# Kernel tuning notes

Hardware: AMD Instinct MI355X
Metric: run time of the kernel (lower is better)

Reference implementation:

```python
import jax, jax.numpy as jnp
import numpy as np

VOCAB, EMBED, HIDDEN, NCLS = 50257, 64, 64, 5
B, S = 4096, 512
BN_EPS = 1e-5


def setup_inputs() -> dict:
    key = jax.random.key(0)
    ks = jax.random.split(key, 10)
    x = jax.random.randint(ks[0], (B, S), 0, VOCAB, dtype=jnp.int64 if jax.config.jax_enable_x64 else jnp.int32)
    emb = jax.random.normal(ks[1], (VOCAB, EMBED), dtype=jnp.float32)
    emb = emb.at[0].set(0.0)  # padding_idx=0
    s = 1.0 / np.sqrt(HIDDEN)
    W_ih = jax.random.uniform(ks[2], (HIDDEN, EMBED), minval=-s, maxval=s, dtype=jnp.float32)
    W_hh = jax.random.uniform(ks[3], (HIDDEN, HIDDEN), minval=-s, maxval=s, dtype=jnp.float32)
    b_ih = jax.random.uniform(ks[4], (HIDDEN,), minval=-s, maxval=s, dtype=jnp.float32)
    b_hh = jax.random.uniform(ks[5], (HIDDEN,), minval=-s, maxval=s, dtype=jnp.float32)
    gamma = jnp.ones((HIDDEN,), dtype=jnp.float32)
    beta = jnp.zeros((HIDDEN,), dtype=jnp.float32)
    sf = 1.0 / np.sqrt(HIDDEN)
    W_fc = jax.random.uniform(ks[6], (NCLS, HIDDEN), minval=-sf, maxval=sf, dtype=jnp.float32)
    b_fc = jax.random.uniform(ks[7], (NCLS,), minval=-sf, maxval=sf, dtype=jnp.float32)
    return {"x": x, "emb": emb, "W_ih": W_ih, "W_hh": W_hh, "b_ih": b_ih,
            "b_hh": b_hh, "gamma": gamma, "beta": beta, "W_fc": W_fc, "b_fc": b_fc}


def reference(x, emb, W_ih, W_hh, b_ih, b_hh, gamma, beta, W_fc, b_fc):
    # embedding gather: [B, S, E]
    xe = emb[x]
    # precompute input projection once: [B, S, H] -> scan over time as [S, B, H]
    xp = jnp.einsum('bse,he->bsh', xe, W_ih) + b_ih + b_hh
    xp_t = jnp.swapaxes(xp, 0, 1)

    def step(h, xt):
        h = jnp.tanh(xt + h @ W_hh.T)
        return h, None

    h0 = jnp.zeros((x.shape[0], HIDDEN), dtype=xp.dtype)
    h_n, _ = jax.lax.scan(step, h0, xp_t)

    # BatchNorm1d (training-mode math: batch stats, biased variance)
    mean = jnp.mean(h_n, axis=0)
    var = jnp.mean((h_n - mean) ** 2, axis=0)
    h_bn = (h_n - mean) * jax.lax.rsqrt(var + BN_EPS) * gamma + beta
    # dropout is identity in eval / deterministic reference
    logits = h_bn @ W_fc.T + b_fc  # [B, 5]
    return logits
```

## Files before the change

kernel.cpp:

```cpp
#include <hip/hip_runtime.h>

typedef unsigned short u16;
typedef __attribute__((ext_vector_type(8))) short bf16x8;
typedef __attribute__((ext_vector_type(4))) float f32x4;
typedef __attribute__((ext_vector_type(4))) u16 u16x4;

constexpr int BATCH  = 4096;
constexpr int SEQ    = 512;
constexpr int HID    = 64;
constexpr int EMB_N4 = 50257 * 64 / 4;

__device__ __forceinline__ float bf2f(u16 u) {
  union { unsigned int i; float f; } c; c.i = ((unsigned int)u) << 16; return c.f;
}
__device__ __forceinline__ u16 f2bf(float f) {
  union { float f; unsigned int i; } c; c.f = f;
  unsigned int u = c.i;
  u += 0x7fffu + ((u >> 16) & 1u);
  return (u16)(u >> 16);
}

#define MFMA16(a, b, c) __builtin_amdgcn_mfma_f32_16x16x32_bf16(a, b, c, 0, 0, 0)

__global__ __launch_bounds__(256) void prep_kernel(
    const float4* __restrict__ emb4, const float* __restrict__ Wih,
    const float* __restrict__ Whh, u16x4* __restrict__ emb_bf4,
    u16* __restrict__ wih_hi, u16* __restrict__ whh_hi, u16* __restrict__ whh_lo,
    float* __restrict__ bn_acc)
{
  int gid = blockIdx.x * 256 + threadIdx.x;
  if (gid < EMB_N4) {
    float4 v = emb4[gid];
    u16x4 o;
    o.x = f2bf(v.x); o.y = f2bf(v.y); o.z = f2bf(v.z); o.w = f2bf(v.w);
    emb_bf4[gid] = o;
  } else if (gid < EMB_N4 + 1024) {
    int i0 = (gid - EMB_N4) * 4;
    #pragma unroll
    for (int k = 0; k < 4; ++k) {
      int i = i0 + k;
      wih_hi[i] = f2bf(Wih[i]);
      float w = Whh[i];
      u16 hi = f2bf(w);
      whh_hi[i] = hi;
      whh_lo[i] = f2bf(w - bf2f(hi));
    }
  } else if (gid < EMB_N4 + 1024 + 128) {
    bn_acc[gid - (EMB_N4 + 1024)] = 0.f;
  }
}

__global__ __launch_bounds__(256, 1) void rnn_scan_kernel(
    const int* __restrict__ xx, const u16* __restrict__ emb_bf,
    const u16* __restrict__ wih_hi, const u16* __restrict__ whh_hi,
    const u16* __restrict__ whh_lo,
    const float* __restrict__ b_ih, const float* __restrict__ b_hh,
    float* __restrict__ hT , float* __restrict__ bn_acc)
{
  __shared__ u16 hbuf[2 * 2048];
  const int tid = threadIdx.x;
  const int w = tid >> 6;
  const int L = tid & 63;
  const int n = L & 15;
  const int q = L >> 4;
  const int R0 = blockIdx.x << 4;
  const int row  = R0 + n;
  const int feat = (w << 4) + n;

  ((int4*)hbuf)[tid] = int4{0, 0, 0, 0};

  bf16x8 Bih0 = *(const bf16x8*)(wih_hi + feat * 64 +      8 * q);
  bf16x8 Bih1 = *(const bf16x8*)(wih_hi + feat * 64 + 32 + 8 * q);
  bf16x8 Bh0  = *(const bf16x8*)(whh_hi + feat * 64 +      8 * q);
  bf16x8 Bh1  = *(const bf16x8*)(whh_hi + feat * 64 + 32 + 8 * q);
  bf16x8 Bl0  = *(const bf16x8*)(whh_lo + feat * 64 +      8 * q);
  bf16x8 Bl1  = *(const bf16x8*)(whh_lo + feat * 64 + 32 + 8 * q);
  const float bias = b_ih[feat] + b_hh[feat];

  const int r0off = n * 64 + (((0 + q) ^ (n & 7)) << 3);
  const int r1off = n * 64 + (((4 + q) ^ (n & 7)) << 3);
  const int cwbase = (w << 1) + (n >> 3);

  const int4* x4 = (const int4*)(xx + row * SEQ);
  int4 K1 = x4[1];

  bf16x8 e0[4], e1[4];
  {
    int4 K0 = x4[0];
    const int id0[4] = {K0.x, K0.y, K0.z, K0.w};
    #pragma unroll
    for (int u = 0; u < 4; ++u) {
      const u16* eb = emb_bf + (long)id0[u] * 64 + 8 * q;
      e0[u] = *(const bf16x8*)(eb);
      e1[u] = *(const bf16x8*)(eb + 32);
    }
  }

  __syncthreads();

  for (int t = 0; t < SEQ / 4; ++t) {
    int4 K2 = x4[(t + 2 < SEQ / 4) ? t + 2 : SEQ / 4 - 1];
    const int nid[4] = {K1.x, K1.y, K1.z, K1.w};
    const bool lastt = (t == SEQ / 4 - 1);

    #pragma unroll
    for (int u = 0; u < 4; ++u) {
      const int p = u & 1;
      const u16* hb = hbuf + p * 2048;
      bf16x8 ah0 = *(const bf16x8*)(hb + r0off);
      bf16x8 ah1 = *(const bf16x8*)(hb + r1off);
      bf16x8 al0 = *(const bf16x8*)(hb + 1024 + r0off);
      bf16x8 al1 = *(const bf16x8*)(hb + 1024 + r1off);

      f32x4 C1 = {bias, bias, bias, bias};
      C1 = MFMA16(e0[u], Bih0, C1);
      C1 = MFMA16(e1[u], Bih1, C1);

      {
        const u16* eb = emb_bf + (long)nid[u] * 64 + 8 * q;
        e0[u] = *(const bf16x8*)(eb);
        e1[u] = *(const bf16x8*)(eb + 32);
      }

      f32x4 Cx = {0.f, 0.f, 0.f, 0.f};
      f32x4 Cy = {0.f, 0.f, 0.f, 0.f};
      f32x4 Cz = {0.f, 0.f, 0.f, 0.f};
      Cx = MFMA16(ah0, Bh0, Cx);  Cx = MFMA16(al0, Bh0, Cx);
      Cy = MFMA16(ah1, Bh1, Cy);  Cy = MFMA16(al1, Bh1, Cy);
      Cz = MFMA16(ah0, Bl0, Cz);  Cz = MFMA16(ah1, Bl1, Cz);

      u16* wb = hbuf + (p ^ 1) * 2048;
      float th4[4];
      #pragma unroll
      for (int r = 0; r < 4; ++r) {
        float v = (C1[r] + Cx[r]) + (Cy[r] + Cz[r]);
        float ex = __builtin_amdgcn_exp2f(2.8853900817779268f * v);
        float th = fmaf(-2.0f, __builtin_amdgcn_rcpf(ex + 1.0f), 1.0f);
        th4[r] = th;
        const int mw = (q << 2) + r;
        const int off = mw * 64 + ((cwbase ^ (mw & 7)) << 3) + (n & 7);
        unsigned int tb = __float_as_uint(th);
        wb[off] = (u16)(tb >> 16);
        wb[1024 + off] = (u16)(__float_as_uint(th - __uint_as_float(tb & 0xffff0000u)) >> 16);
      }

      if (u == 3 && lastt) {
        float s1 = 0.f, s2 = 0.f;
        #pragma unroll
        for (int r = 0; r < 4; ++r) {
          hT[feat * BATCH + R0 + (q << 2) + r] = th4[r];
          s1 += th4[r];
          s2 = fmaf(th4[r], th4[r], s2);
        }
        s1 += __shfl_xor(s1, 16, 64);  s2 += __shfl_xor(s2, 16, 64);
        s1 += __shfl_xor(s1, 32, 64);  s2 += __shfl_xor(s2, 32, 64);
        if (q == 0) {
          atomicAdd(bn_acc + feat, s1);
          atomicAdd(bn_acc + 64 + feat, s2);
        }
      }

      asm volatile("s_waitcnt lgkmcnt(0)\n\ts_barrier" ::: "memory");
    }
    K1 = K2;
  }
}

__global__ __launch_bounds__(256) void head_kernel(
    const float* __restrict__ hT, const float* __restrict__ bn_acc,
    const float* __restrict__ gamma, const float* __restrict__ beta,
    const float* __restrict__ Wfc, const float* __restrict__ bfc,
    float* __restrict__ out)
{
  __shared__ float sc[64], sh[64];
  const int tid = threadIdx.x;
  if (tid < 64) {
    float mean = bn_acc[tid] * (1.0f / BATCH);
    float var  = bn_acc[64 + tid] * (1.0f / BATCH) - mean * mean;
    float inv  = rsqrtf(var + 1e-5f);
    float s    = gamma[tid] * inv;
    sc[tid] = s;
    sh[tid] = beta[tid] - mean * s;
  }
  __syncthreads();
  const int b = blockIdx.x * 256 + tid;
  float acc[5];
  #pragma unroll
  for (int c = 0; c < 5; ++c) acc[c] = bfc[c];
  for (int j = 0; j < HID; ++j) {
    float hv  = hT[j * BATCH + b];
    float hat = fmaf(hv, sc[j], sh[j]);
    #pragma unroll
    for (int c = 0; c < 5; ++c) acc[c] = fmaf(hat, Wfc[c * 64 + j], acc[c]);
  }
  #pragma unroll
  for (int c = 0; c < 5; ++c) out[b * 5 + c] = acc[c];
}

extern "C" void kernel_launch(void* const* d_in, const int* in_sizes, int n_in,
                              void* d_out, int out_size, void* d_ws, size_t ws_size,
                              hipStream_t stream)
{
  const int*   x     = (const int*)d_in[0];
  const float* emb   = (const float*)d_in[1];
  const float* W_ih  = (const float*)d_in[2];
  const float* W_hh  = (const float*)d_in[3];
  const float* b_ih  = (const float*)d_in[4];
  const float* b_hh  = (const float*)d_in[5];
  const float* gamma = (const float*)d_in[6];
  const float* beta  = (const float*)d_in[7];
  const float* W_fc  = (const float*)d_in[8];
  const float* b_fc  = (const float*)d_in[9];

  char* ws = (char*)d_ws;
  float* hT     = (float*)ws;
  float* bn_acc = (float*)(ws + 1048576);
  u16*   emb_bf = (u16*)(ws + 1049088);
  u16*   wih_hi = (u16*)(ws + 7481984);
  u16*   whh_hi = (u16*)(ws + 7490176);
  u16*   whh_lo = (u16*)(ws + 7498368);

  const int prep_items = EMB_N4 + 1024 + 128;
  prep_kernel<<<dim3((prep_items + 255) / 256), dim3(256), 0, stream>>>(
      (const float4*)emb, W_ih, W_hh, (u16x4*)emb_bf, wih_hi, whh_hi, whh_lo, bn_acc);
  rnn_scan_kernel<<<dim3(BATCH / 16), dim3(256), 0, stream>>>(
      x, emb_bf, wih_hi, whh_hi, whh_lo, b_ih, b_hh, hT, bn_acc);
  head_kernel<<<dim3(BATCH / 256), dim3(256), 0, stream>>>(
      hT, bn_acc, gamma, beta, W_fc, b_fc, (float*)d_out);
}
```

Measured before the change: 251.5 us.

## Run RNN scan in one wave with register-resident fp16 hidden state

Restructures the recurrent scan so that a single 64-lane wavefront owns all 64 hidden features for 16 batch rows. The transposed MFMA output layout is fed back directly as the next step's B operand, which removes the LDS hidden-state buffer and the per-timestep barrier. It also replaces the split bf16 hi/lo operands with single fp16 operands and folds the tanh exp2 scaling into the weights and bias. This halves the MFMA count per step and removes the shared-memory traffic on the critical path. The costs are lower hidden-state precision, now fp16 without error compensation, and only one wave per block, which reduces latency hiding across the 256 blocks.

```diff
diff --git a/kernel.cpp b/kernel.cpp
--- a/kernel.cpp
+++ b/kernel.cpp
@@ -1,102 +1,90 @@
 #include <hip/hip_runtime.h>
 
-typedef unsigned short u16;
-typedef __attribute__((ext_vector_type(8))) short bf16x8;
+typedef _Float16 f16;
+typedef __attribute__((ext_vector_type(4))) _Float16 f16x4;
+typedef __attribute__((ext_vector_type(8))) _Float16 f16x8;
 typedef __attribute__((ext_vector_type(4))) float f32x4;
-typedef __attribute__((ext_vector_type(4))) u16 u16x4;
 
 constexpr int BATCH  = 4096;
 constexpr int SEQ    = 512;
 constexpr int HID    = 64;
 constexpr int EMB_N4 = 50257 * 64 / 4;
-
-__device__ __forceinline__ float bf2f(u16 u) {
-  union { unsigned int i; float f; } c; c.i = ((unsigned int)u) << 16; return c.f;
-}
-__device__ __forceinline__ u16 f2bf(float f) {
-  union { float f; unsigned int i; } c; c.f = f;
-  unsigned int u = c.i;
-  u += 0x7fffu + ((u >> 16) & 1u);
-  return (u16)(u >> 16);
-}
-
-#define MFMA16(a, b, c) __builtin_amdgcn_mfma_f32_16x16x32_bf16(a, b, c, 0, 0, 0)
+constexpr float LOG2E2 = 2.8853900817779268f;
+
+#define MFMA_K32(a, b, c) __builtin_amdgcn_mfma_f32_16x16x32_f16(a, b, c, 0, 0, 0)
 
 __global__ __launch_bounds__(256) void prep_kernel(
     const float4* __restrict__ emb4, const float* __restrict__ Wih,
-    const float* __restrict__ Whh, u16x4* __restrict__ emb_bf4,
-    u16* __restrict__ wih_hi, u16* __restrict__ whh_hi, u16* __restrict__ whh_lo,
-    float* __restrict__ bn_acc)
+    const float* __restrict__ Whh, f16x4* __restrict__ emb_f4,
+    f16* __restrict__ wih_f, f16* __restrict__ whh_f, float* __restrict__ bn_acc)
 {
   int gid = blockIdx.x * 256 + threadIdx.x;
   if (gid < EMB_N4) {
     float4 v = emb4[gid];
-    u16x4 o;
-    o.x = f2bf(v.x); o.y = f2bf(v.y); o.z = f2bf(v.z); o.w = f2bf(v.w);
-    emb_bf4[gid] = o;
+    f16x4 o = {(f16)v.x, (f16)v.y, (f16)v.z, (f16)v.w};
+    emb_f4[gid] = o;
   } else if (gid < EMB_N4 + 1024) {
     int i0 = (gid - EMB_N4) * 4;
     #pragma unroll
     for (int k = 0; k < 4; ++k) {
       int i = i0 + k;
-      wih_hi[i] = f2bf(Wih[i]);
-      float w = Whh[i];
-      u16 hi = f2bf(w);
-      whh_hi[i] = hi;
-      whh_lo[i] = f2bf(w - bf2f(hi));
+      wih_f[i] = (f16)(Wih[i] * LOG2E2);
+      whh_f[i] = (f16)(Whh[i] * LOG2E2);
     }
   } else if (gid < EMB_N4 + 1024 + 128) {
     bn_acc[gid - (EMB_N4 + 1024)] = 0.f;
   }
 }
 
-__global__ __launch_bounds__(256, 1) void rnn_scan_kernel(
-    const int* __restrict__ xx, const u16* __restrict__ emb_bf,
-    const u16* __restrict__ wih_hi, const u16* __restrict__ whh_hi,
-    const u16* __restrict__ whh_lo,
+__global__ __launch_bounds__(64, 1) void rnn_scan_kernel(
+    const int* __restrict__ xx, const f16* __restrict__ emb,
+    const f16* __restrict__ wih, const f16* __restrict__ whh,
     const float* __restrict__ b_ih, const float* __restrict__ b_hh,
     float* __restrict__ hT , float* __restrict__ bn_acc)
 {
-  __shared__ u16 hbuf[2 * 2048];
-  const int tid = threadIdx.x;
-  const int w = tid >> 6;
-  const int L = tid & 63;
+  const int L = threadIdx.x;
   const int n = L & 15;
   const int q = L >> 4;
   const int R0 = blockIdx.x << 4;
-  const int row  = R0 + n;
-  const int feat = (w << 4) + n;
-
-  ((int4*)hbuf)[tid] = int4{0, 0, 0, 0};
-
-  bf16x8 Bih0 = *(const bf16x8*)(wih_hi + feat * 64 +      8 * q);
-  bf16x8 Bih1 = *(const bf16x8*)(wih_hi + feat * 64 + 32 + 8 * q);
-  bf16x8 Bh0  = *(const bf16x8*)(whh_hi + feat * 64 +      8 * q);
-  bf16x8 Bh1  = *(const bf16x8*)(whh_hi + feat * 64 + 32 + 8 * q);
-  bf16x8 Bl0  = *(const bf16x8*)(whh_lo + feat * 64 +      8 * q);
-  bf16x8 Bl1  = *(const bf16x8*)(whh_lo + feat * 64 + 32 + 8 * q);
-  const float bias = b_ih[feat] + b_hh[feat];
-
-  const int r0off = n * 64 + (((0 + q) ^ (n & 7)) << 3);
-  const int r1off = n * 64 + (((4 + q) ^ (n & 7)) << 3);
-  const int cwbase = (w << 1) + (n >> 3);
-
-  const int4* x4 = (const int4*)(xx + row * SEQ);
+
+  f16x8 Wi[4][2], Wp[4][2];
+  f32x4 bias[4];
+  #pragma unroll
+  for (int f = 0; f < 4; ++f) {
+    const f16* wr = whh + (16 * f + n) * 64;
+    #pragma unroll
+    for (int h = 0; h < 2; ++h) {
+      f16x4 lo = *(const f16x4*)(wr + 32 * h + 4 * q);
+      f16x4 hi = *(const f16x4*)(wr + 32 * h + 16 + 4 * q);
+      Wp[f][h] = __builtin_shufflevector(lo, hi, 0, 1, 2, 3, 4, 5, 6, 7);
+    }
+    const f16* wi = wih + (16 * f + n) * 64;
+    Wi[f][0] = *(const f16x8*)(wi + 8 * q);
+    Wi[f][1] = *(const f16x8*)(wi + 32 + 8 * q);
+    float4 bi = *(const float4*)(b_ih + 16 * f + 4 * q);
+    float4 bh = *(const float4*)(b_hh + 16 * f + 4 * q);
+    f32x4 b = {(bi.x + bh.x) * LOG2E2, (bi.y + bh.y) * LOG2E2,
+               (bi.z + bh.z) * LOG2E2, (bi.w + bh.w) * LOG2E2};
+    bias[f] = b;
+  }
+
+  f16x8 hB01 = {0, 0, 0, 0, 0, 0, 0, 0};
+  f16x8 hB23 = {0, 0, 0, 0, 0, 0, 0, 0};
+
+  const int4* x4 = (const int4*)(xx + (R0 + n) * SEQ);
   int4 K1 = x4[1];
 
-  bf16x8 e0[4], e1[4];
+  f16x8 e0[4], e1[4];
   {
     int4 K0 = x4[0];
     const int id0[4] = {K0.x, K0.y, K0.z, K0.w};
     #pragma unroll
     for (int u = 0; u < 4; ++u) {
-      const u16* eb = emb_bf + (long)id0[u] * 64 + 8 * q;
-      e0[u] = *(const bf16x8*)(eb);
-      e1[u] = *(const bf16x8*)(eb + 32);
-    }
-  }
-
-  __syncthreads();
+      const f16* eb = emb + (long)id0[u] * 64 + 8 * q;
+      e0[u] = *(const f16x8*)(eb);
+      e1[u] = *(const f16x8*)(eb + 32);
+    }
+  }
 
   for (int t = 0; t < SEQ / 4; ++t) {
     int4 K2 = x4[(t + 2 < SEQ / 4) ? t + 2 : SEQ / 4 - 1];
@@ -105,62 +93,67 @@
 
     #pragma unroll
     for (int u = 0; u < 4; ++u) {
-      const int p = u & 1;
-      const u16* hb = hbuf + p * 2048;
-      bf16x8 ah0 = *(const bf16x8*)(hb + r0off);
-      bf16x8 ah1 = *(const bf16x8*)(hb + r1off);
-      bf16x8 al0 = *(const bf16x8*)(hb + 1024 + r0off);
-      bf16x8 al1 = *(const bf16x8*)(hb + 1024 + r1off);
-
-      f32x4 C1 = {bias, bias, bias, bias};
-      C1 = MFMA16(e0[u], Bih0, C1);
-      C1 = MFMA16(e1[u], Bih1, C1);
+      f32x4 D0 = MFMA_K32(Wi[0][0], e0[u], bias[0]);
+      f32x4 D1 = MFMA_K32(Wi[1][0], e0[u], bias[1]);
+      f32x4 D2 = MFMA_K32(Wi[2][0], e0[u], bias[2]);
+      f32x4 D3 = MFMA_K32(Wi[3][0], e0[u], bias[3]);
+      D0 = MFMA_K32(Wi[0][1], e1[u], D0);
+      D1 = MFMA_K32(Wi[1][1], e1[u], D1);
+      D2 = MFMA_K32(Wi[2][1], e1[u], D2);
+      D3 = MFMA_K32(Wi[3][1], e1[u], D3);
 
       {
-        const u16* eb = emb_bf + (long)nid[u] * 64 + 8 * q;
-        e0[u] = *(const bf16x8*)(eb);
-        e1[u] = *(const bf16x8*)(eb + 32);
+        const f16* eb = emb + (long)nid[u] * 64 + 8 * q;
+        e0[u] = *(const f16x8*)(eb);
+        e1[u] = *(const f16x8*)(eb + 32);
       }
 
-      f32x4 Cx = {0.f, 0.f, 0.f, 0.f};
-      f32x4 Cy = {0.f, 0.f, 0.f, 0.f};
-      f32x4 Cz = {0.f, 0.f, 0.f, 0.f};
-      Cx = MFMA16(ah0, Bh0, Cx);  Cx = MFMA16(al0, Bh0, Cx);
-      Cy = MFMA16(ah1, Bh1, Cy);  Cy = MFMA16(al1, Bh1, Cy);
-      Cz = MFMA16(ah0, Bl0, Cz);  Cz = MFMA16(ah1, Bl1, Cz);
-
-      u16* wb = hbuf + (p ^ 1) * 2048;
-      float th4[4];
+      D0 = MFMA_K32(Wp[0][0], hB01, D0);
+      D1 = MFMA_K32(Wp[1][0], hB01, D1);
+      D2 = MFMA_K32(Wp[2][0], hB01, D2);
+      D3 = MFMA_K32(Wp[3][0], hB01, D3);
+      D0 = MFMA_K32(Wp[0][1], hB23, D0);
+      D1 = MFMA_K32(Wp[1][1], hB23, D1);
+      D2 = MFMA_K32(Wp[2][1], hB23, D2);
+      D3 = MFMA_K32(Wp[3][1], hB23, D3);
+
+      float th[4][4];
       #pragma unroll
       for (int r = 0; r < 4; ++r) {
-        float v = (C1[r] + Cx[r]) + (Cy[r] + Cz[r]);
-        float ex = __builtin_amdgcn_exp2f(2.8853900817779268f * v);
-        float th = fmaf(-2.0f, __builtin_amdgcn_rcpf(ex + 1.0f), 1.0f);
-        th4[r] = th;
-        const int mw = (q << 2) + r;
-        const int off = mw * 64 + ((cwbase ^ (mw & 7)) << 3) + (n & 7);
-        unsigned int tb = __float_as_uint(th);
-        wb[off] = (u16)(tb >> 16);
-        wb[1024 + off] = (u16)(__float_as_uint(th - __uint_as_float(tb & 0xffff0000u)) >> 16);
+        float e0f = __builtin_amdgcn_exp2f(D0[r]);
+        float e1f = __builtin_amdgcn_exp2f(D1[r]);
+        float e2f = __builtin_amdgcn_exp2f(D2[r]);
+        float e3f = __builtin_amdgcn_exp2f(D3[r]);
+        th[0][r] = fmaf(-2.0f, __builtin_amdgcn_rcpf(e0f + 1.0f), 1.0f);
+        th[1][r] = fmaf(-2.0f, __builtin_amdgcn_rcpf(e1f + 1.0f), 1.0f);
+        th[2][r] = fmaf(-2.0f, __builtin_amdgcn_rcpf(e2f + 1.0f), 1.0f);
+        th[3][r] = fmaf(-2.0f, __builtin_amdgcn_rcpf(e3f + 1.0f), 1.0f);
+        hB01[r]     = (f16)th[0][r];
+        hB01[4 + r] = (f16)th[1][r];
+        hB23[r]     = (f16)th[2][r];
+        hB23[4 + r] = (f16)th[3][r];
       }
 
-      if (u == 3 && lastt) {
-        float s1 = 0.f, s2 = 0.f;
+      if (lastt && u == 3) {
         #pragma unroll
-        for (int r = 0; r < 4; ++r) {
-          hT[feat * BATCH + R0 + (q << 2) + r] = th4[r];
-          s1 += th4[r];
-          s2 = fmaf(th4[r], th4[r], s2);
-        }
-        s1 += __shfl_xor(s1, 16, 64);  s2 += __shfl_xor(s2, 16, 64);
-        s1 += __shfl_xor(s1, 32, 64);  s2 += __shfl_xor(s2, 32, 64);
-        if (q == 0) {
-          atomicAdd(bn_acc + feat, s1);
-          atomicAdd(bn_acc + 64 + feat, s2);
+        for (int f = 0; f < 4; ++f) {
+          #pragma unroll
+          for (int r = 0; r < 4; ++r) {
+            float v = th[f][r];
+            const int feat = 16 * f + 4 * q + r;
+            hT[feat * BATCH + R0 + n] = v;
+            float s1 = v, s2 = v * v;
+            s1 += __shfl_xor(s1, 1, 64);  s2 += __shfl_xor(s2, 1, 64);
+            s1 += __shfl_xor(s1, 2, 64);  s2 += __shfl_xor(s2, 2, 64);
+            s1 += __shfl_xor(s1, 4, 64);  s2 += __shfl_xor(s2, 4, 64);
+            s1 += __shfl_xor(s1, 8, 64);  s2 += __shfl_xor(s2, 8, 64);
+            if (n == 0) {
+              atomicAdd(bn_acc + feat, s1);
+              atomicAdd(bn_acc + 64 + feat, s2);
+            }
+          }
         }
       }
-
-      asm volatile("s_waitcnt lgkmcnt(0)\n\ts_barrier" ::: "memory");
     }
     K1 = K2;
   }
@@ -215,16 +208,15 @@
   char* ws = (char*)d_ws;
   float* hT     = (float*)ws;
   float* bn_acc = (float*)(ws + 1048576);
-  u16*   emb_bf = (u16*)(ws + 1049088);
-  u16*   wih_hi = (u16*)(ws + 7481984);
-  u16*   whh_hi = (u16*)(ws + 7490176);
-  u16*   whh_lo = (u16*)(ws + 7498368);
+  f16*   emb_f  = (f16*)(ws + 1049088);
+  f16*   wih_f  = (f16*)(ws + 7481984);
+  f16*   whh_f  = (f16*)(ws + 7490176);
 
   const int prep_items = EMB_N4 + 1024 + 128;
   prep_kernel<<<dim3((prep_items + 255) / 256), dim3(256), 0, stream>>>(
-      (const float4*)emb, W_ih, W_hh, (u16x4*)emb_bf, wih_hi, whh_hi, whh_lo, bn_acc);
-  rnn_scan_kernel<<<dim3(BATCH / 16), dim3(256), 0, stream>>>(
-      x, emb_bf, wih_hi, whh_hi, whh_lo, b_ih, b_hh, hT, bn_acc);
+      (const float4*)emb, W_ih, W_hh, (f16x4*)emb_f, wih_f, whh_f, bn_acc);
+  rnn_scan_kernel<<<dim3(BATCH / 16), dim3(64), 0, stream>>>(
+      x, emb_f, wih_f, whh_f, b_ih, b_hh, hT, bn_acc);
   head_kernel<<<dim3(BATCH / 256), dim3(256), 0, stream>>>(
       hT, bn_acc, gamma, beta, W_fc, b_fc, (float*)d_out);
 }
```

After: 284.7 us. 1.13x slower.
